# Kernel tuning notes

Hardware: AMD Instinct MI355X
Metric: run time of the kernel (lower is better)

Reference implementation:

```python
import jax, jax.numpy as jnp
import numpy as np

B, L, D, H, DFF, WS = 8, 16384, 256, 8, 1024, 32
HD = D // H
NW = L // WS


def setup_inputs() -> dict:
    key = jax.random.key(0)
    ks = jax.random.split(key, 12)
    p = lambda k, sh: jax.random.normal(k, sh, jnp.float32) * 0.02
    return {
        "query_em": jax.random.normal(ks[0], (B, L, D), jnp.float32),
        "key_value_em": jax.random.normal(ks[1], (B, L, D), jnp.float32),
        "Wq": p(ks[2], (D, D)), "bq": jnp.zeros((D,), jnp.float32),
        "Wk": p(ks[3], (D, D)), "bk": jnp.zeros((D,), jnp.float32),
        "Wv": p(ks[4], (D, D)), "bv": jnp.zeros((D,), jnp.float32),
        "Wo": p(ks[5], (D, D)), "bo": jnp.zeros((D,), jnp.float32),
        "g1": jnp.ones((D,), jnp.float32), "be1": jnp.zeros((D,), jnp.float32),
        "W1": p(ks[6], (D, DFF)), "bf1": jnp.zeros((DFF,), jnp.float32),
        "W2": p(ks[7], (DFF, D)), "bf2": jnp.zeros((D,), jnp.float32),
        "g2": jnp.ones((D,), jnp.float32), "be2": jnp.zeros((D,), jnp.float32),
    }


def _layernorm(x, g, b):
    m = jnp.mean(x, axis=-1, keepdims=True)
    v = jnp.var(x, axis=-1, keepdims=True)
    return (x - m) * jax.lax.rsqrt(v + 1e-5) * g + b


def _encoder_layer(q, kv, Wq, bq, Wk, bk, Wv, bv, Wo, bo, g1, be1, W1, bf1, W2, bf2, g2, be2):
    # q, kv: [B, NW, WS, D] -- attention only within each window of WS tokens
    b, nw, ws, d = q.shape
    qh = (q @ Wq + bq).reshape(b, nw, ws, H, HD)
    kh = (kv @ Wk + bk).reshape(b, nw, ws, H, HD)
    vh = (kv @ Wv + bv).reshape(b, nw, ws, H, HD)
    scores = jnp.einsum("bnqhd,bnkhd->bnhqk", qh, kh) / np.sqrt(HD).astype(np.float32)
    attn = jax.nn.softmax(scores, axis=-1)
    o = jnp.einsum("bnhqk,bnkhd->bnqhd", attn, vh).reshape(b, nw, ws, d)
    o = o @ Wo + bo
    x = _layernorm(q + o, g1, be1)  # post-LN residual
    f = jax.nn.relu(x @ W1 + bf1) @ W2 + bf2
    return _layernorm(x + f, g2, be2)


def reference(query_em, key_value_em, Wq, bq, Wk, bk, Wv, bv, Wo, bo,
              g1, be1, W1, bf1, W2, bf2, g2, be2):
    params = (Wq, bq, Wk, bk, Wv, bv, Wo, bo, g1, be1, W1, bf1, W2, bf2, g2, be2)
    q = query_em.reshape(B, NW, WS, D)
    kv = key_value_em.reshape(B, NW, WS, D)
    x = _encoder_layer(q, kv, *params)
    # cyclic shift by half a window-count along the window axis, second pass, shift back
    x = jnp.roll(x, -WS // 2, axis=1)
    x = _encoder_layer(x, x, *params)
    x = jnp.roll(x, WS // 2, axis=1)
    return x.reshape(B, L, D)
```

## Files before the change

### kernel.cpp

```cpp
#include <hip/hip_runtime.h>
#include <cstdint>
#include <cstddef>

typedef unsigned short u16;
typedef __bf16 bf16x8 __attribute__((ext_vector_type(8)));
typedef float f32x4 __attribute__((ext_vector_type(4)));
typedef unsigned short u16x8 __attribute__((ext_vector_type(8)));
typedef unsigned short u16x4 __attribute__((ext_vector_type(4)));

__device__ __forceinline__ u16 f2bf(float f) {
  union { float f; unsigned u; } x; x.f = f;
  unsigned r = x.u + 0x7fffu + ((x.u >> 16) & 1u);
  return (u16)(r >> 16);
}
__device__ __forceinline__ float bf2f(u16 u) {
  union { unsigned u; float f; } x; x.u = ((unsigned)u) << 16;
  return x.f;
}
__device__ __forceinline__ void gload16(const void* g, void* l) {
  __builtin_amdgcn_global_load_lds(
      (const __attribute__((address_space(1))) unsigned int*)g,
      (__attribute__((address_space(3))) unsigned int*)l, 16, 0, 0);
}

template<int MODE>
__global__ __launch_bounds__(256) void gemm_bt(
    const u16* __restrict__ Ab, int lda, const u16* __restrict__ Bt,
    const float* __restrict__ bias, u16* __restrict__ C0, int ldc, int coff,
    u16* __restrict__ C2, int vsplit, int N, int K, int gy)
{
  __shared__ u16 As[2 * 128 * 32];
  __shared__ u16 Bs[2 * 128 * 32];
  const int tid  = threadIdx.x;
  const int lane = tid & 63, w = tid >> 6;
  const int nwg = gridDim.x, o = blockIdx.x;
  const int lid = (o & 7) * (nwg >> 3) + (o >> 3);
  const int by = lid % gy, bx = lid / gy;
  const int row0 = bx * 128, col0 = by * 128;
  const int wr = (w >> 1) * 64, wc = (w & 1) * 64;
  const int fr = lane & 15, fg = lane >> 4;
  const int srow  = (w << 5) + (lane >> 2);
  const int sslot = (lane & 3) ^ ((lane >> 2) & 3);
  const int AB = 128 * 32;

  auto stageB = [&](int buf, int k0) {
    #pragma unroll
    for (int h = 0; h < 2; ++h)
      gload16((const char*)Bt + ((size_t)(col0 + srow + h*16) * K + k0) * 2 + sslot*16,
              &Bs[buf*AB + ((w << 5) + h*16) * 32]);
  };
  auto stageA16 = [&](int buf, int k0) {
    #pragma unroll
    for (int h = 0; h < 2; ++h)
      gload16((const char*)Ab + ((size_t)(row0 + srow + h*16) * lda + k0) * 2 + sslot*16,
              &As[buf*AB + ((w << 5) + h*16) * 32]);
  };

  f32x4 acc[4][4] = {};

  stageA16(0, 0); stageB(0, 0);
  __syncthreads();
  int cur = 0;
  for (int k0 = 0; k0 < K; k0 += 32) {
    if (k0 + 32 < K) { stageA16(cur ^ 1, k0 + 32); stageB(cur ^ 1, k0 + 32); }
    bf16x8 af[4], bf[4];
    #pragma unroll
    for (int i = 0; i < 4; ++i) {
      const int r = wr + i*16 + fr;
      af[i] = *(const bf16x8*)&As[cur*AB + r*32 + ((fg ^ (fr & 3)) << 3)];
    }
    #pragma unroll
    for (int j = 0; j < 4; ++j) {
      const int r = wc + j*16 + fr;
      bf[j] = *(const bf16x8*)&Bs[cur*AB + r*32 + ((fg ^ (fr & 3)) << 3)];
    }
    #pragma unroll
    for (int i = 0; i < 4; ++i)
      #pragma unroll
      for (int j = 0; j < 4; ++j)
        acc[i][j] = __builtin_amdgcn_mfma_f32_16x16x32_bf16(af[i], bf[j], acc[i][j], 0, 0, 0);
    __syncthreads();
    cur ^= 1;
  }

  const int vpart = (MODE == 2 && col0 >= vsplit);
  #pragma unroll
  for (int j = 0; j < 4; ++j) {
    const int c  = col0 + wc + j*16 + fr;
    const float bv = bias[c];
    #pragma unroll
    for (int i = 0; i < 4; ++i) {
      if (vpart) {
        const int cv = c - vsplit;
        const int rb = row0 + wr + i*16 + fg*4;
        u16x4 vv;
        #pragma unroll
        for (int t = 0; t < 4; ++t) vv[t] = f2bf(acc[i][j][t] + bv);
        *(u16x4*)&C2[((size_t)(rb >> 5) * 256 + cv) * 32 + (rb & 31)] = vv;
      } else {
        #pragma unroll
        for (int t = 0; t < 4; ++t) {
          const int r = row0 + wr + i*16 + fg*4 + t;
          C0[(size_t)r * ldc + coff + c] = f2bf(acc[i][j][t] + bv);
        }
      }
    }
  }
}

__device__ __forceinline__ void gemm_f32_pipe(
    const float* __restrict__ Af, int lda, const u16* __restrict__ Bt,
    const float* __restrict__ bias, u16* __restrict__ C0, int ldc, int coff,
    u16* __restrict__ C2, int vsplit, int N, int K, int gy, int nwg, int o,
    u16* As, u16* Bs)
{
  const int tid  = threadIdx.x;
  const int lane = tid & 63, w = tid >> 6;
  const int lid = (o & 7) * (nwg >> 3) + (o >> 3);
  const int by = lid % gy, bx = lid / gy;
  const int row0 = bx * 128, col0 = by * 128;
  const int wr = (w >> 1) * 64, wc = (w & 1) * 64;
  const int fr = lane & 15, fg = lane >> 4;
  const int srow  = (w << 5) + (lane >> 2);
  const int sslot = (lane & 3) ^ ((lane >> 2) & 3);
  const int AB = 128 * 32;
  const int NT = K >> 5;

  auto stageB = [&](int buf, int k0) {
    #pragma unroll
    for (int h = 0; h < 2; ++h)
      gload16((const char*)Bt + ((size_t)(col0 + srow + h*16) * K + k0) * 2 + sslot*16,
              &Bs[buf*AB + ((w << 5) + h*16) * 32]);
  };
  f32x4 pre[2][2][2];
  auto loadA32 = [&](int set, int k0) {
    #pragma unroll
    for (int p = 0; p < 2; ++p) {
      const int sidx = tid + p*256, rr = sidx >> 2, sl = sidx & 3;
      const float* src = &Af[(size_t)(row0 + rr) * lda + k0 + sl*8];
      pre[set][p][0] = *(const f32x4*)src;
      pre[set][p][1] = *(const f32x4*)(src + 4);
    }
  };
  auto writeA32 = [&](int set, int buf) {
    #pragma unroll
    for (int p = 0; p < 2; ++p) {
      const int sidx = tid + p*256, rr = sidx >> 2, sl = sidx & 3;
      u16x8 ov = { f2bf(pre[set][p][0][0]), f2bf(pre[set][p][0][1]),
                   f2bf(pre[set][p][0][2]), f2bf(pre[set][p][0][3]),
                   f2bf(pre[set][p][1][0]), f2bf(pre[set][p][1][1]),
                   f2bf(pre[set][p][1][2]), f2bf(pre[set][p][1][3]) };
      *(u16x8*)&As[buf*AB + rr*32 + ((sl ^ (rr & 3)) << 3)] = ov;
    }
  };

  f32x4 acc[4][4] = {};

  loadA32(0, 0);
  loadA32(1, 32);
  stageB(0, 0);
  asm volatile("s_waitcnt vmcnt(6)" ::: "memory");
  writeA32(0, 0);
  asm volatile("s_waitcnt lgkmcnt(0)" ::: "memory");
  __builtin_amdgcn_s_barrier();
  __builtin_amdgcn_sched_barrier(0);
  stageB(1, 32);

  for (int j = 0; j < NT; ++j) {
    if (j + 2 < NT) loadA32(j & 1, (j + 2) << 5);
    if (j + 2 < NT)      asm volatile("s_waitcnt vmcnt(6)" ::: "memory");
    else if (j + 1 < NT) asm volatile("s_waitcnt vmcnt(2)" ::: "memory");
    else                 asm volatile("s_waitcnt vmcnt(0)" ::: "memory");
    if (j + 1 < NT) {
      writeA32((j + 1) & 1, (j + 1) % 3);
      asm volatile("s_waitcnt lgkmcnt(0)" ::: "memory");
    }
    __builtin_amdgcn_s_barrier();
    __builtin_amdgcn_sched_barrier(0);
    if (j + 2 < NT) stageB((j + 2) % 3, (j + 2) << 5);
    const int cb = j % 3;
    bf16x8 af[4], bf[4];
    #pragma unroll
    for (int i = 0; i < 4; ++i) {
      const int r = wr + i*16 + fr;
      af[i] = *(const bf16x8*)&As[cb*AB + r*32 + ((fg ^ (fr & 3)) << 3)];
    }
    #pragma unroll
    for (int j2 = 0; j2 < 4; ++j2) {
      const int r = wc + j2*16 + fr;
      bf[j2] = *(const bf16x8*)&Bs[cb*AB + r*32 + ((fg ^ (fr & 3)) << 3)];
    }
    #pragma unroll
    for (int i = 0; i < 4; ++i)
      #pragma unroll
      for (int j2 = 0; j2 < 4; ++j2)
        acc[i][j2] = __builtin_amdgcn_mfma_f32_16x16x32_bf16(af[i], bf[j2], acc[i][j2], 0, 0, 0);
  }

  const int vpart = (col0 >= vsplit);
  #pragma unroll
  for (int j = 0; j < 4; ++j) {
    const int c  = col0 + wc + j*16 + fr;
    const float bv = bias[c];
    #pragma unroll
    for (int i = 0; i < 4; ++i) {
      if (vpart) {
        const int cv = c - vsplit;
        const int rb = row0 + wr + i*16 + fg*4;
        u16x4 vv;
        #pragma unroll
        for (int t = 0; t < 4; ++t) vv[t] = f2bf(acc[i][j][t] + bv);
        *(u16x4*)&C2[((size_t)(rb >> 5) * 256 + cv) * 32 + (rb & 31)] = vv;
      } else {
        #pragma unroll
        for (int t = 0; t < 4; ++t) {
          const int r = row0 + wr + i*16 + fg*4 + t;
          C0[(size_t)r * ldc + coff + c] = f2bf(acc[i][j][t] + bv);
        }
      }
    }
  }
}

__global__ __launch_bounds__(256) void gemm_l1(
    const float* __restrict__ query, const float* __restrict__ keyval,
    const u16* __restrict__ WqkvT, const float* __restrict__ bq,
    const float* __restrict__ bkv, u16* __restrict__ QKc,
    u16* __restrict__ Vtc)
{
  __shared__ u16 As[3 * 128 * 32];
  __shared__ u16 Bs[3 * 128 * 32];
  const int o = blockIdx.x;
  if (o < 2048) {
    gemm_f32_pipe(query, 256, WqkvT, bq, QKc, 512, 0, Vtc, 1 << 30,
                  256, 256, 2, 2048, o, As, Bs);
  } else {
    gemm_f32_pipe(keyval, 256, WqkvT + 65536, bkv, QKc, 512, 256, Vtc, 256,
                  512, 256, 4, 4096, o - 2048, As, Bs);
  }
}

template<int RES_F32>
__global__ __launch_bounds__(512) void gemm_oln(
    const u16* __restrict__ Ap, int lda, const u16* __restrict__ Bt,
    const float* __restrict__ bias, const void* __restrict__ Res,
    const float* __restrict__ g, const float* __restrict__ be,
    u16* __restrict__ Y, int K)
{
  __shared__ u16 As[2][128 * 32];
  __shared__ u16 Bs[2][256 * 32];
  __shared__ float2 red[128][4];
  __shared__ float2 stats[128];
  const int tid  = threadIdx.x;
  const int lane = tid & 63, w = tid >> 6;
  const int nwg = gridDim.x, o = blockIdx.x;
  const int lid = (o & 7) * (nwg >> 3) + (o >> 3);
  const int row0 = lid * 128;
  const int wr = (w >> 2) * 64, wc = (w & 3) * 64;
  const int fr = lane & 15, fg = lane >> 4;
  const int sr   = lane >> 2;
  const int sslot = (lane & 3) ^ ((lane >> 2) & 3);

  auto stage = [&](int buf, int k0) {
    gload16((const char*)Ap + ((size_t)(row0 + (w << 4) + sr) * lda + k0) * 2 + sslot*16,
            &As[buf][((w << 4)) * 32]);
    #pragma unroll
    for (int h = 0; h < 2; ++h)
      gload16((const char*)Bt + ((size_t)((w << 5) + h*16 + sr) * K + k0) * 2 + sslot*16,
              &Bs[buf][((w << 5) + h*16) * 32]);
  };

  f32x4 acc[4][4] = {};

  stage(0, 0);
  __syncthreads();
  int cur = 0;
  for (int k0 = 0; k0 < K; k0 += 32) {
    if (k0 + 32 < K) stage(cur ^ 1, k0 + 32);
    bf16x8 af[4], bf[4];
    #pragma unroll
    for (int i = 0; i < 4; ++i) {
      const int r = wr + i*16 + fr;
      af[i] = *(const bf16x8*)&As[cur][r*32 + ((fg ^ (fr & 3)) << 3)];
    }
    #pragma unroll
    for (int j = 0; j < 4; ++j) {
      const int r = wc + j*16 + fr;
      bf[j] = *(const bf16x8*)&Bs[cur][r*32 + ((fg ^ (fr & 3)) << 3)];
    }
    #pragma unroll
    for (int i = 0; i < 4; ++i)
      #pragma unroll
      for (int j = 0; j < 4; ++j)
        acc[i][j] = __builtin_amdgcn_mfma_f32_16x16x32_bf16(af[i], bf[j], acc[i][j], 0, 0, 0);
    __syncthreads();
    cur ^= 1;
  }

  float ps[4][4] = {}, pq[4][4] = {};
  #pragma unroll
  for (int j = 0; j < 4; ++j) {
    const int c = wc + j*16 + fr;
    const float bv = bias[c];
    #pragma unroll
    for (int i = 0; i < 4; ++i) {
      #pragma unroll
      for (int t = 0; t < 4; ++t) {
        const int r = row0 + wr + i*16 + fg*4 + t;
        const float rv = RES_F32 ? ((const float*)Res)[(size_t)r * 256 + c]
                                 : bf2f(((const u16*)Res)[(size_t)r * 256 + c]);
        float v = acc[i][j][t] + bv + rv;
        acc[i][j][t] = v;
        ps[i][t] += v;
        pq[i][t] += v * v;
      }
    }
  }
  #pragma unroll
  for (int d = 1; d < 16; d <<= 1) {
    #pragma unroll
    for (int i = 0; i < 4; ++i)
      #pragma unroll
      for (int t = 0; t < 4; ++t) {
        ps[i][t] += __shfl_xor(ps[i][t], d, 64);
        pq[i][t] += __shfl_xor(pq[i][t], d, 64);
      }
  }
  if (fr == 0) {
    #pragma unroll
    for (int i = 0; i < 4; ++i)
      #pragma unroll
      for (int t = 0; t < 4; ++t)
        red[wr + i*16 + fg*4 + t][w & 3] = make_float2(ps[i][t], pq[i][t]);
  }
  __syncthreads();
  if (tid < 128) {
    float S = 0.f, Q = 0.f;
    #pragma unroll
    for (int ww = 0; ww < 4; ++ww) { float2 p = red[tid][ww]; S += p.x; Q += p.y; }
    const float m = S * (1.f/256.f);
    const float var = Q * (1.f/256.f) - m*m;
    stats[tid] = make_float2(m, rsqrtf(var + 1e-5f));
  }
  __syncthreads();
  #pragma unroll
  for (int i = 0; i < 4; ++i) {
    #pragma unroll
    for (int t = 0; t < 4; ++t) {
      const int rl = wr + i*16 + fg*4 + t;
      const float2 st = stats[rl];
      const size_t r = row0 + rl;
      #pragma unroll
      for (int j = 0; j < 4; ++j) {
        const int c = wc + j*16 + fr;
        Y[r * 256 + c] = f2bf((acc[i][j][t] - st.x) * st.y * g[c] + be[c]);
      }
    }
  }
}

template<int OUT_F32>
__global__ __launch_bounds__(512, 2) void ffn_fused(
    const u16* __restrict__ X, const u16* __restrict__ W1T,
    const float* __restrict__ b1, const u16* __restrict__ W2T,
    const float* __restrict__ b2, const float* __restrict__ g,
    const float* __restrict__ be, void* __restrict__ Y)
{
  __shared__ u16 W1s[4][32 * 256];
  __shared__ u16 W2s[4][256 * 32];
  __shared__ u16 Hs[8][32 * 32];
  __shared__ float b1s[1024];
  const int tid = threadIdx.x, lane = tid & 63, w = tid >> 6;
  const int fr = lane & 15, fg = lane >> 4;
  const int row0 = blockIdx.x * 256 + w * 32;
  u16* Hw = &Hs[w][0];
  const int hxor = (fr >> 1) & 3;

  auto stage = [&](int buf, int hb) {
    #pragma unroll
    for (int h = 0; h < 2; ++h) {
      const int r = w*4 + h*2 + (lane >> 5);
      const int sl = (lane & 31) ^ (r & 7);
      gload16((const char*)W1T + ((size_t)((hb << 5) + r) * 256 + sl*8) * 2,
              &W1s[buf][(w*4 + h*2) * 256]);
    }
    #pragma unroll
    for (int h = 0; h < 2; ++h) {
      const int r = w*32 + h*16 + (lane >> 2);
      const int sl = (lane & 3) ^ ((r >> 1) & 3);
      gload16((const char*)W2T + ((size_t)r * 1024 + (hb << 5) + sl*8) * 2,
              &W2s[buf][(w*32 + h*16) * 32]);
    }
  };

  if (tid < 256) {
    f32x4 bv = *(const f32x4*)&b1[tid * 4];
    *(f32x4*)&b1s[tid * 4] = bv;
  }
  bf16x8 af[2][8];
  #pragma unroll
  for (int g2 = 0; g2 < 2; ++g2)
    #pragma unroll
    for (int kf = 0; kf < 8; ++kf)
      af[g2][kf] = *(const bf16x8*)&X[(size_t)(row0 + g2*16 + fr) * 256 + kf*32 + fg*8];
  asm volatile("s_waitcnt vmcnt(0)" ::: "memory");

  f32x4 acc2[2][16] = {};

  auto compute_slice = [&](int hb, int cur) {
    f32x4 acc1[2][2] = {};
    #pragma unroll
    for (int kf = 0; kf < 8; ++kf) {
      #pragma unroll
      for (int hf = 0; hf < 2; ++hf) {
        const int n = hf*16 + fr;
        bf16x8 w1f = *(const bf16x8*)&W1s[cur][n*256 + ((((kf << 2) | fg) ^ (n & 7)) << 3)];
        acc1[hf][0] = __builtin_amdgcn_mfma_f32_16x16x32_bf16(w1f, af[0][kf], acc1[hf][0], 0, 0, 0);
        acc1[hf][1] = __builtin_amdgcn_mfma_f32_16x16x32_bf16(w1f, af[1][kf], acc1[hf][1], 0, 0, 0);
      }
    }
    #pragma unroll
    for (int g2 = 0; g2 < 2; ++g2) {
      #pragma unroll
      for (int hf = 0; hf < 2; ++hf) {
        const int h0 = hf*16 + fg*4;
        f32x4 b4 = *(const f32x4*)&b1s[(hb << 5) + h0];
        u16x4 hv;
        #pragma unroll
        for (int t = 0; t < 4; ++t) {
          float v = acc1[hf][g2][t] + b4[t];
          hv[t] = f2bf(v > 0.f ? v : 0.f);
        }
        const int tok = g2*16 + fr;
        *(u16x4*)((char*)Hw + tok*64 + ((((hf << 1) | (fg >> 1)) ^ hxor) << 4)
                                     + ((fg & 1) << 3)) = hv;
      }
    }
    asm volatile("s_waitcnt lgkmcnt(0)" ::: "memory");
    __builtin_amdgcn_sched_barrier(0);

    bf16x8 hf2[2];
    #pragma unroll
    for (int g2 = 0; g2 < 2; ++g2) {
      const int tok = g2*16 + fr;
      hf2[g2] = *(const bf16x8*)((char*)Hw + tok*64 + ((fg ^ hxor) << 4));
    }
    #pragma unroll
    for (int nf = 0; nf < 16; ++nf) {
      const int n = nf*16 + fr;
      bf16x8 w2f = *(const bf16x8*)&W2s[cur][n*32 + ((fg ^ ((n >> 1) & 3)) << 3)];
      acc2[0][nf] = __builtin_amdgcn_mfma_f32_16x16x32_bf16(hf2[0], w2f, acc2[0][nf], 0, 0, 0);
      acc2[1][nf] = __builtin_amdgcn_mfma_f32_16x16x32_bf16(hf2[1], w2f, acc2[1][nf], 0, 0, 0);
    }
  };

  stage(0, 0);
  stage(1, 1);
  for (int hb = 0; hb < 30; ++hb) {
    stage((hb + 2) & 3, hb + 2);
    asm volatile("s_waitcnt vmcnt(8)" ::: "memory");
    __builtin_amdgcn_s_barrier();
    __builtin_amdgcn_sched_barrier(0);
    compute_slice(hb, hb & 3);
  }
  asm volatile("s_waitcnt vmcnt(4)" ::: "memory");
  __builtin_amdgcn_s_barrier();
  __builtin_amdgcn_sched_barrier(0);
  compute_slice(30, 30 & 3);
  asm volatile("s_waitcnt vmcnt(0)" ::: "memory");
  __builtin_amdgcn_s_barrier();
  __builtin_amdgcn_sched_barrier(0);
  compute_slice(31, 31 & 3);

  #pragma unroll
  for (int g2 = 0; g2 < 2; ++g2) {
    const int rbase = row0 + g2*16 + fg*4;
    float s1[4] = {}, sq[4] = {};
    #pragma unroll
    for (int nf = 0; nf < 16; ++nf) {
      const int c = nf*16 + fr;
      const float b = b2[c];
      #pragma unroll
      for (int t = 0; t < 4; ++t) {
        float v = acc2[g2][nf][t] + b + bf2f(X[(size_t)(rbase + t) * 256 + c]);
        acc2[g2][nf][t] = v;
        s1[t] += v; sq[t] += v * v;
      }
    }
    #pragma unroll
    for (int d = 1; d < 16; d <<= 1) {
      #pragma unroll
      for (int t = 0; t < 4; ++t) {
        s1[t] += __shfl_xor(s1[t], d, 64);
        sq[t] += __shfl_xor(sq[t], d, 64);
      }
    }
    float mean[4], rstd[4];
    #pragma unroll
    for (int t = 0; t < 4; ++t) {
      mean[t] = s1[t] * (1.f/256.f);
      const float var = sq[t] * (1.f/256.f) - mean[t]*mean[t];
      rstd[t] = rsqrtf(var + 1e-5f);
    }
    #pragma unroll
    for (int nf = 0; nf < 16; ++nf) {
      const int c = nf*16 + fr;
      const float gc = g[c], bc = be[c];
      #pragma unroll
      for (int t = 0; t < 4; ++t) {
        const float y = (acc2[g2][nf][t] - mean[t]) * rstd[t] * gc + bc;
        if (OUT_F32) ((float*)Y)[(size_t)(rbase + t) * 256 + c] = y;
        else         ((u16*)Y)[(size_t)(rbase + t) * 256 + c] = f2bf(y);
      }
    }
  }
}

__global__ __launch_bounds__(256) void attn_mfma(
    const u16* Q, int sq, const u16* __restrict__ K, int sk,
    const u16* __restrict__ Vt, u16* O, int so)
{
  __shared__ u16 P[4][32 * 40];
  const int tid = threadIdx.x, lane = tid & 63, w = tid >> 6;
  const int win = blockIdx.x * 4 + w;
  const size_t q0 = (size_t)win * 32;
  const int fr = lane & 15, fg = lane >> 4;
  u16* Pw = &P[w][0];
  const float scale = 0.17677669529663687f;

  for (int h = 0; h < 8; ++h) {
    const int co = h * 32;
    bf16x8 qa[2], kb[2];
    #pragma unroll
    for (int i = 0; i < 2; ++i)
      qa[i] = *(const bf16x8*)&Q[(q0 + i*16 + fr) * sq + co + fg*8];
    #pragma unroll
    for (int j = 0; j < 2; ++j)
      kb[j] = *(const bf16x8*)&K[(q0 + j*16 + fr) * sk + co + fg*8];
    f32x4 s[2][2] = {};
    #pragma unroll
    for (int i = 0; i < 2; ++i)
      #pragma unroll
      for (int j = 0; j < 2; ++j)
        s[i][j] = __builtin_amdgcn_mfma_f32_16x16x32_bf16(qa[i], kb[j], s[i][j], 0, 0, 0);

    float inv[2][4];
    #pragma unroll
    for (int i = 0; i < 2; ++i) {
      #pragma unroll
      for (int t = 0; t < 4; ++t) {
        float a0 = s[i][0][t] * scale, a1 = s[i][1][t] * scale;
        float mx = fmaxf(a0, a1);
        #pragma unroll
        for (int d = 1; d < 16; d <<= 1) mx = fmaxf(mx, __shfl_xor(mx, d, 64));
        const float p0 = __expf(a0 - mx), p1 = __expf(a1 - mx);
        float sm = p0 + p1;
        #pragma unroll
        for (int d = 1; d < 16; d <<= 1) sm += __shfl_xor(sm, d, 64);
        inv[i][t] = 1.f / sm;
        const int q = i*16 + fg*4 + t;
        Pw[q*40 + fr]      = f2bf(p0);
        Pw[q*40 + 16 + fr] = f2bf(p1);
      }
    }

    bf16x8 pa[2], vb[2];
    #pragma unroll
    for (int i = 0; i < 2; ++i)
      pa[i] = *(const bf16x8*)&Pw[(i*16 + fr)*40 + fg*8];
    #pragma unroll
    for (int j = 0; j < 2; ++j)
      vb[j] = *(const bf16x8*)&Vt[(size_t)win*8192 + (co + j*16 + fr)*32 + fg*8];
    f32x4 oacc[2][2] = {};
    #pragma unroll
    for (int i = 0; i < 2; ++i)
      #pragma unroll
      for (int j = 0; j < 2; ++j)
        oacc[i][j] = __builtin_amdgcn_mfma_f32_16x16x32_bf16(pa[i], vb[j], oacc[i][j], 0, 0, 0);

    #pragma unroll
    for (int i = 0; i < 2; ++i)
      #pragma unroll
      for (int j = 0; j < 2; ++j)
        #pragma unroll
        for (int t = 0; t < 4; ++t)
          O[(q0 + i*16 + fg*4 + t) * so + co + j*16 + fr] =
              f2bf(oacc[i][j][t] * inv[i][t]);
  }
}

__global__ __launch_bounds__(256) void wprep_all(
    const float* __restrict__ Wq, const float* __restrict__ Wk,
    const float* __restrict__ Wv, const float* __restrict__ Wo,
    const float* __restrict__ W1, const float* __restrict__ W2,
    const float* __restrict__ bq, const float* __restrict__ bk,
    const float* __restrict__ bv,
    u16* __restrict__ WqkvT, u16* __restrict__ WoT,
    u16* __restrict__ W1T, u16* __restrict__ W2T, float* __restrict__ bqkv)
{
  const int b = blockIdx.x, t = threadIdx.x;
  if (b < 1024) {
    const int which = b >> 8, idx = ((b & 255) << 8) + t;
    const float* W = which == 0 ? Wq : which == 1 ? Wk : which == 2 ? Wv : Wo;
    u16* Wt = which == 3 ? WoT : WqkvT + which * 65536;
    const int k = idx >> 8, n = idx & 255;
    Wt[n * 256 + k] = f2bf(W[idx]);
  } else if (b < 2048) {
    const int idx = ((b - 1024) << 8) + t;
    const int k = idx >> 10, n = idx & 1023;
    W1T[n * 256 + k] = f2bf(W1[idx]);
  } else if (b < 3072) {
    const int idx = ((b - 2048) << 8) + t;
    const int k = idx >> 8, n = idx & 255;
    W2T[n * 1024 + k] = f2bf(W2[idx]);
  } else {
    const int i = ((b - 3072) << 8) + t;
    bqkv[i] = i < 256 ? bq[i] : (i < 512 ? bk[i - 256] : bv[i - 512]);
  }
}

extern "C" void kernel_launch(void* const* d_in, const int* in_sizes, int n_in,
                              void* d_out, int out_size, void* d_ws, size_t ws_size,
                              hipStream_t stream)
{
  const float* query  = (const float*)d_in[0];
  const float* keyval = (const float*)d_in[1];
  const float* Wq = (const float*)d_in[2];  const float* bq  = (const float*)d_in[3];
  const float* Wk = (const float*)d_in[4];  const float* bk  = (const float*)d_in[5];
  const float* Wv = (const float*)d_in[6];  const float* bv  = (const float*)d_in[7];
  const float* Wo = (const float*)d_in[8];  const float* bo  = (const float*)d_in[9];
  const float* g1 = (const float*)d_in[10]; const float* be1 = (const float*)d_in[11];
  const float* W1 = (const float*)d_in[12]; const float* bf1 = (const float*)d_in[13];
  const float* W2 = (const float*)d_in[14]; const float* bf2 = (const float*)d_in[15];
  const float* g2 = (const float*)d_in[16]; const float* be2 = (const float*)d_in[17];

  const int M = 131072;
  char* ws = (char*)d_ws;
  u16*  xcur = (u16*)ws;
  u16*  x1   = (u16*)(ws + (64ull  << 20));
  u16*  QKc  = (u16*)(ws + (256ull << 20));
  u16*  Vtc  = (u16*)(ws + (384ull << 20));
  u16*  WqkvT = (u16*)(ws + (448ull << 20));
  u16*  WoT   = WqkvT + 196608;
  u16*  W1T   = WoT   + 65536;
  u16*  W2T   = W1T   + 262144;
  float* bqkv = (float*)(W2T + 262144);
  float* bkv  = bqkv + 256;

  wprep_all<<<3075, 256, 0, stream>>>(Wq, Wk, Wv, Wo, W1, W2, bq, bk, bv,
                                      WqkvT, WoT, W1T, W2T, bqkv);


  gemm_l1<<<6144, 256, 0, stream>>>(query, keyval, WqkvT, bq, bkv, QKc, Vtc);
  attn_mfma<<<1024, 256, 0, stream>>>(QKc, 512, QKc + 256, 512, Vtc, QKc, 512);
  gemm_oln<1><<<1024, 512, 0, stream>>>(
      QKc, 512, WoT, bo, query, g1, be1, x1, 256);
  ffn_fused<0><<<512, 512, 0, stream>>>(
      x1, W1T, bf1, W2T, bf2, g2, be2, xcur);

  gemm_bt<2><<<6144, 256, 0, stream>>>(
      xcur, 256, WqkvT, bqkv, QKc, 512, 0, Vtc, 512, 768, 256, 6);
  attn_mfma<<<1024, 256, 0, stream>>>(QKc, 512, QKc + 256, 512, Vtc, QKc, 512);
  gemm_oln<0><<<1024, 512, 0, stream>>>(
      QKc, 512, WoT, bo, xcur, g1, be1, x1, 256);
  ffn_fused<1><<<512, 512, 0, stream>>>(
      x1, W1T, bf1, W2T, bf2, g2, be2, d_out);
}
```

Before: 881.2 us.

## Widen first-layer QKV GEMM tiles to full 256 columns with 512 threads

Restructures the first-layer fused QKV projection so each workgroup computes a 128x256 tile covering a full Q, K or V output, using 512 threads and 3072 blocks instead of 128x128 tiles with 256 threads. Each fp32 activation row is then loaded and converted to bf16 once per segment rather than twice, which cuts global reads of the input. The hand-tuned triple-buffered pipeline with explicit waitcnts is replaced by a simpler double-buffered loop with __syncthreads, which may expose more memory latency.

```diff
diff --git a/kernel.cpp b/kernel.cpp
--- a/kernel.cpp
+++ b/kernel.cpp
@@ -108,135 +108,106 @@
   }
 }
 
-__device__ __forceinline__ void gemm_f32_pipe(
-    const float* __restrict__ Af, int lda, const u16* __restrict__ Bt,
-    const float* __restrict__ bias, u16* __restrict__ C0, int ldc, int coff,
-    u16* __restrict__ C2, int vsplit, int N, int K, int gy, int nwg, int o,
-    u16* As, u16* Bs)
+__global__ __launch_bounds__(512) void gemm_l1(
+    const float* __restrict__ query, const float* __restrict__ keyval,
+    const u16* __restrict__ WqkvT, const float* __restrict__ bqkv,
+    u16* __restrict__ QKc, u16* __restrict__ Vtc)
 {
-  const int tid  = threadIdx.x;
-  const int lane = tid & 63, w = tid >> 6;
-  const int lid = (o & 7) * (nwg >> 3) + (o >> 3);
-  const int by = lid % gy, bx = lid / gy;
-  const int row0 = bx * 128, col0 = by * 128;
-  const int wr = (w >> 1) * 64, wc = (w & 1) * 64;
+  __shared__ u16 As[2][128 * 32];
+  __shared__ u16 Bs[2][256 * 32];
+  const int tid = threadIdx.x, lane = tid & 63, w = tid >> 6;
+  const int o = blockIdx.x;
+  const int seg = o >> 10, ob = o & 1023;
+  const int lid = (ob & 7) * 128 + (ob >> 3);
+  const int row0 = lid * 128;
+  const float* Af = (seg == 0) ? query : keyval;
+  const u16* Bt = WqkvT + seg * 65536;
+  const float* bias = bqkv + seg * 256;
+  const int wr = (w >> 2) * 64, wc = (w & 3) * 64;
   const int fr = lane & 15, fg = lane >> 4;
-  const int srow  = (w << 5) + (lane >> 2);
+  const int sr = lane >> 2;
   const int sslot = (lane & 3) ^ ((lane >> 2) & 3);
-  const int AB = 128 * 32;
-  const int NT = K >> 5;
+  const int arr = tid >> 2, asl = tid & 3;
 
   auto stageB = [&](int buf, int k0) {
     #pragma unroll
     for (int h = 0; h < 2; ++h)
-      gload16((const char*)Bt + ((size_t)(col0 + srow + h*16) * K + k0) * 2 + sslot*16,
-              &Bs[buf*AB + ((w << 5) + h*16) * 32]);
-  };
-  f32x4 pre[2][2][2];
-  auto loadA32 = [&](int set, int k0) {
-    #pragma unroll
-    for (int p = 0; p < 2; ++p) {
-      const int sidx = tid + p*256, rr = sidx >> 2, sl = sidx & 3;
-      const float* src = &Af[(size_t)(row0 + rr) * lda + k0 + sl*8];
-      pre[set][p][0] = *(const f32x4*)src;
-      pre[set][p][1] = *(const f32x4*)(src + 4);
-    }
-  };
-  auto writeA32 = [&](int set, int buf) {
-    #pragma unroll
-    for (int p = 0; p < 2; ++p) {
-      const int sidx = tid + p*256, rr = sidx >> 2, sl = sidx & 3;
-      u16x8 ov = { f2bf(pre[set][p][0][0]), f2bf(pre[set][p][0][1]),
-                   f2bf(pre[set][p][0][2]), f2bf(pre[set][p][0][3]),
-                   f2bf(pre[set][p][1][0]), f2bf(pre[set][p][1][1]),
-                   f2bf(pre[set][p][1][2]), f2bf(pre[set][p][1][3]) };
-      *(u16x8*)&As[buf*AB + rr*32 + ((sl ^ (rr & 3)) << 3)] = ov;
-    }
+      gload16((const char*)Bt + ((size_t)((w << 5) + h*16 + sr) * 256 + k0) * 2 + sslot*16,
+              &Bs[buf][((w << 5) + h*16) * 32]);
+  };
+  f32x4 pre0, pre1;
+  auto loadA32 = [&](int k0) {
+    const float* src = &Af[(size_t)(row0 + arr) * 256 + k0 + asl*8];
+    pre0 = *(const f32x4*)src;
+    pre1 = *(const f32x4*)(src + 4);
+  };
+  auto writeA32 = [&](int buf) {
+    u16x8 ov = { f2bf(pre0[0]), f2bf(pre0[1]), f2bf(pre0[2]), f2bf(pre0[3]),
+                 f2bf(pre1[0]), f2bf(pre1[1]), f2bf(pre1[2]), f2bf(pre1[3]) };
+    *(u16x8*)&As[buf][arr*32 + ((asl ^ (arr & 3)) << 3)] = ov;
   };
 
   f32x4 acc[4][4] = {};
 
-  loadA32(0, 0);
-  loadA32(1, 32);
-  stageB(0, 0);
-  asm volatile("s_waitcnt vmcnt(6)" ::: "memory");
-  writeA32(0, 0);
-  asm volatile("s_waitcnt lgkmcnt(0)" ::: "memory");
-  __builtin_amdgcn_s_barrier();
-  __builtin_amdgcn_sched_barrier(0);
-  stageB(1, 32);
-
-  for (int j = 0; j < NT; ++j) {
-    if (j + 2 < NT) loadA32(j & 1, (j + 2) << 5);
-    if (j + 2 < NT)      asm volatile("s_waitcnt vmcnt(6)" ::: "memory");
-    else if (j + 1 < NT) asm volatile("s_waitcnt vmcnt(2)" ::: "memory");
-    else                 asm volatile("s_waitcnt vmcnt(0)" ::: "memory");
-    if (j + 1 < NT) {
-      writeA32((j + 1) & 1, (j + 1) % 3);
-      asm volatile("s_waitcnt lgkmcnt(0)" ::: "memory");
-    }
-    __builtin_amdgcn_s_barrier();
-    __builtin_amdgcn_sched_barrier(0);
-    if (j + 2 < NT) stageB((j + 2) % 3, (j + 2) << 5);
-    const int cb = j % 3;
+  loadA32(0); stageB(0, 0); writeA32(0);
+  __syncthreads();
+  int cur = 0;
+  for (int k0 = 0; k0 < 256; k0 += 32) {
+    const int has_next = (k0 + 32 < 256);
+    if (has_next) {
+      loadA32(k0 + 32);
+      stageB(cur ^ 1, k0 + 32);
+    }
     bf16x8 af[4], bf[4];
     #pragma unroll
     for (int i = 0; i < 4; ++i) {
       const int r = wr + i*16 + fr;
-      af[i] = *(const bf16x8*)&As[cb*AB + r*32 + ((fg ^ (fr & 3)) << 3)];
-    }
-    #pragma unroll
-    for (int j2 = 0; j2 < 4; ++j2) {
-      const int r = wc + j2*16 + fr;
-      bf[j2] = *(const bf16x8*)&Bs[cb*AB + r*32 + ((fg ^ (fr & 3)) << 3)];
+      af[i] = *(const bf16x8*)&As[cur][r*32 + ((fg ^ (fr & 3)) << 3)];
+    }
+    #pragma unroll
+    for (int j = 0; j < 4; ++j) {
+      const int r = wc + j*16 + fr;
+      bf[j] = *(const bf16x8*)&Bs[cur][r*32 + ((fg ^ (fr & 3)) << 3)];
     }
     #pragma unroll
     for (int i = 0; i < 4; ++i)
       #pragma unroll
-      for (int j2 = 0; j2 < 4; ++j2)
-        acc[i][j2] = __builtin_amdgcn_mfma_f32_16x16x32_bf16(af[i], bf[j2], acc[i][j2], 0, 0, 0);
-  }
-
-  const int vpart = (col0 >= vsplit);
-  #pragma unroll
-  for (int j = 0; j < 4; ++j) {
-    const int c  = col0 + wc + j*16 + fr;
-    const float bv = bias[c];
-    #pragma unroll
-    for (int i = 0; i < 4; ++i) {
-      if (vpart) {
-        const int cv = c - vsplit;
+      for (int j = 0; j < 4; ++j)
+        acc[i][j] = __builtin_amdgcn_mfma_f32_16x16x32_bf16(af[i], bf[j], acc[i][j], 0, 0, 0);
+    if (has_next) writeA32(cur ^ 1);
+    __syncthreads();
+    cur ^= 1;
+  }
+
+  if (seg == 2) {
+    #pragma unroll
+    for (int j = 0; j < 4; ++j) {
+      const int c = wc + j*16 + fr;
+      const float bv = bias[c];
+      #pragma unroll
+      for (int i = 0; i < 4; ++i) {
         const int rb = row0 + wr + i*16 + fg*4;
         u16x4 vv;
         #pragma unroll
         for (int t = 0; t < 4; ++t) vv[t] = f2bf(acc[i][j][t] + bv);
-        *(u16x4*)&C2[((size_t)(rb >> 5) * 256 + cv) * 32 + (rb & 31)] = vv;
-      } else {
+        *(u16x4*)&Vtc[((size_t)(rb >> 5) * 256 + c) * 32 + (rb & 31)] = vv;
+      }
+    }
+  } else {
+    const int coff = seg * 256;
+    #pragma unroll
+    for (int j = 0; j < 4; ++j) {
+      const int c = wc + j*16 + fr;
+      const float bv = bias[c];
+      #pragma unroll
+      for (int i = 0; i < 4; ++i) {
         #pragma unroll
         for (int t = 0; t < 4; ++t) {
           const int r = row0 + wr + i*16 + fg*4 + t;
-          C0[(size_t)r * ldc + coff + c] = f2bf(acc[i][j][t] + bv);
+          QKc[(size_t)r * 512 + coff + c] = f2bf(acc[i][j][t] + bv);
         }
       }
     }
-  }
-}
-
-__global__ __launch_bounds__(256) void gemm_l1(
-    const float* __restrict__ query, const float* __restrict__ keyval,
-    const u16* __restrict__ WqkvT, const float* __restrict__ bq,
-    const float* __restrict__ bkv, u16* __restrict__ QKc,
-    u16* __restrict__ Vtc)
-{
-  __shared__ u16 As[3 * 128 * 32];
-  __shared__ u16 Bs[3 * 128 * 32];
-  const int o = blockIdx.x;
-  if (o < 2048) {
-    gemm_f32_pipe(query, 256, WqkvT, bq, QKc, 512, 0, Vtc, 1 << 30,
-                  256, 256, 2, 2048, o, As, Bs);
-  } else {
-    gemm_f32_pipe(keyval, 256, WqkvT + 65536, bkv, QKc, 512, 256, Vtc, 256,
-                  512, 256, 4, 4096, o - 2048, As, Bs);
   }
 }
 
@@ -645,13 +616,12 @@
   u16*  W1T   = WoT   + 65536;
   u16*  W2T   = W1T   + 262144;
   float* bqkv = (float*)(W2T + 262144);
-  float* bkv  = bqkv + 256;
 
   wprep_all<<<3075, 256, 0, stream>>>(Wq, Wk, Wv, Wo, W1, W2, bq, bk, bv,
                                       WqkvT, WoT, W1T, W2T, bqkv);
 
 
-  gemm_l1<<<6144, 256, 0, stream>>>(query, keyval, WqkvT, bq, bkv, QKc, Vtc);
+  gemm_l1<<<3072, 512, 0, stream>>>(query, keyval, WqkvT, bqkv, QKc, Vtc);
   attn_mfma<<<1024, 256, 0, stream>>>(QKc, 512, QKc + 256, 512, Vtc, QKc, 512);
   gemm_oln<1><<<1024, 512, 0, stream>>>(
       QKc, 512, WoT, bo, query, g1, be1, x1, 256);
```

Result: faster. 853.0 us (-3.2%).
